# Kernel tuning notes

Measured on AMD Instinct MI355X. Metric: run time of the kernel, lower is better.

Reference implementation:

```python
import jax, jax.numpy as jnp
import numpy as np

NUM_SEGMENTS = 24  # static max number of sentence segments (matches segment_ids fill_max)


def setup_inputs() -> dict:
    key = jax.random.key(0)
    k1, k2, k3 = jax.random.split(key, 3)
    B, L, S, D = 32, 4, 512, 768
    embeddings = jax.random.normal(k1, (B, L, S, D), dtype=jnp.float32)
    # word index of each subword token (sorted, as produced by left-to-right '##' merging)
    token_group_ids = jnp.sort(jax.random.randint(k2, (B, S), 0, 300), axis=1).astype(jnp.int32)
    # sentence-segment id of each (aggregated) word position (sorted, from '.'-cumsum)
    segment_ids = jnp.sort(jax.random.randint(k3, (B, S), 0, NUM_SEGMENTS), axis=1).astype(jnp.int32)
    return {"embeddings": embeddings, "token_group_ids": token_group_ids, "segment_ids": segment_ids}


def _segsum(data, seg_ids, num_segments):
    # data: [S, D], seg_ids: [S] -> [num_segments, D]
    return jax.ops.segment_sum(data, seg_ids, num_segments=num_segments)


def reference(embeddings, token_group_ids, segment_ids):
    B, L, S, D = embeddings.shape
    # --- aggregate_tokens: scatter-sum subword embeddings into word slots, padded to S ---
    # vmap over batch and layer; word capacity = S (original pads agg_embs back to num_words)
    per_layer = jax.vmap(_segsum, in_axes=(0, None, None))          # over L
    per_batch = jax.vmap(per_layer, in_axes=(0, 0, None))           # over B
    word_layer = per_batch(embeddings, token_group_ids, S)          # [B, L, S, D]
    # --- sentence embedding: mean over (padded) word axis, then sum over layers ---
    sent_embeddings = word_layer.mean(axis=2).sum(axis=1)           # [B, D]
    # --- word embedding: sum over layers (aggregate_method='sum') ---
    word_embeddings = word_layer.sum(axis=1)                        # [B, S, D]
    # --- aggregate_segments: scatter-sum word embeddings into sentence segments ---
    seg_embeddings = jax.vmap(_segsum, in_axes=(0, 0, None))(
        word_embeddings, segment_ids, NUM_SEGMENTS)                 # [B, G, D]
    seg_num = segment_ids.max(axis=1) + 1                           # [B]
    seg_mask = jnp.arange(NUM_SEGMENTS)[None, :] >= seg_num[:, None]  # True = padded segment
    return word_embeddings, sent_embeddings, seg_embeddings, seg_mask
```

## Files before the change

kernel.cpp:

```cpp
#include <hip/hip_runtime.h>

#define BB 32
#define LL 4
#define SS 512
#define DD 768
#define D4 (DD / 4)
#define GG 24

typedef float floatx4 __attribute__((ext_vector_type(4)));

#define WB_STRIDE (SS + 1)
#define SB_STRIDE (GG + 1)

__global__ __launch_bounds__(SS) void bounds_kernel(
    const int* __restrict__ tg, const int* __restrict__ sg,
    int* __restrict__ wb, int* __restrict__ sb)
{
    __shared__ int ltg[SS];
    __shared__ int lsg[SS];
    const int b = blockIdx.x;
    const int t = threadIdx.x;
    ltg[t] = tg[b * SS + t];
    lsg[t] = sg[b * SS + t];
    __syncthreads();

    {
        int v = t, lo = 0, hi = SS;
        while (lo < hi) { int m = (lo + hi) >> 1; if (ltg[m] < v) lo = m + 1; else hi = m; }
        wb[b * WB_STRIDE + t] = lo;
        if (t == 0) wb[b * WB_STRIDE + SS] = SS;
    }
    if (t <= GG) {
        int v = t, lo = 0, hi = SS;
        while (lo < hi) { int m = (lo + hi) >> 1; if (lsg[m] < v) lo = m + 1; else hi = m; }
        sb[b * SB_STRIDE + t] = lo;
    }
}

__global__ __launch_bounds__(D4) void word_agg_kernel(
    const floatx4* __restrict__ emb, const int* __restrict__ wb, floatx4* __restrict__ word)
{
    const int g = blockIdx.x;
    const int b = blockIdx.y;
    const int lo = wb[b * WB_STRIDE + g];
    const int hi = wb[b * WB_STRIDE + g + 1];
    const int d = threadIdx.x;

    floatx4 acc = (floatx4)(0.f);
    for (int s = lo; s < hi; ++s) {
#pragma unroll
        for (int l = 0; l < LL; ++l) {
            floatx4 v = __builtin_nontemporal_load(
                &emb[((size_t)((b * LL + l) * SS + s)) * D4 + d]);
            acc += v;
        }
    }
    word[((size_t)(b * SS + g)) * D4 + d] = acc;
}

__global__ __launch_bounds__(D4) void seg_agg_kernel(
    const floatx4* __restrict__ word, const int* __restrict__ sb, floatx4* __restrict__ seg)
{
    const int t = blockIdx.x;
    const int b = blockIdx.y;
    const int lo = sb[b * SB_STRIDE + t];
    const int hi = sb[b * SB_STRIDE + t + 1];
    const int d = threadIdx.x;

    floatx4 acc = (floatx4)(0.f);
    for (int g = lo; g < hi; ++g) {
        acc += word[((size_t)(b * SS + g)) * D4 + d];
    }
    seg[((size_t)(b * GG + t)) * D4 + d] = acc;
}

__global__ __launch_bounds__(D4) void sent_mask_kernel(
    const floatx4* __restrict__ seg, const int* __restrict__ sg,
    floatx4* __restrict__ sent, float* __restrict__ mask)
{
    const int b = blockIdx.x;
    const int d = threadIdx.x;

    floatx4 acc = (floatx4)(0.f);
#pragma unroll
    for (int t = 0; t < GG; ++t) {
        acc += seg[((size_t)(b * GG + t)) * D4 + d];
    }
    acc *= (1.0f / (float)SS);
    sent[(size_t)b * D4 + d] = acc;

    if (d < GG) {
        const int seg_num = sg[b * SS + (SS - 1)] + 1;
        mask[b * GG + d] = (d >= seg_num) ? 1.0f : 0.0f;
    }
}

extern "C" void kernel_launch(void* const* d_in, const int* in_sizes, int n_in,
                              void* d_out, int out_size, void* d_ws, size_t ws_size,
                              hipStream_t stream) {
    const float* emb = (const float*)d_in[0];
    const int*   tg  = (const int*)d_in[1];
    const int*   sg  = (const int*)d_in[2];

    float* out  = (float*)d_out;
    float* word = out;
    float* sent = word + (size_t)BB * SS * DD;
    float* seg  = sent + (size_t)BB * DD;
    float* mask = seg  + (size_t)BB * GG * DD;

    int* wb = (int*)d_ws;
    int* sb = wb + BB * WB_STRIDE;

    bounds_kernel<<<BB, SS, 0, stream>>>(tg, sg, wb, sb);
    word_agg_kernel<<<dim3(SS, BB), D4, 0, stream>>>((const floatx4*)emb, wb, (floatx4*)word);
    seg_agg_kernel<<<dim3(GG, BB), D4, 0, stream>>>((const floatx4*)word, sb, (floatx4*)seg);
    sent_mask_kernel<<<BB, D4, 0, stream>>>((const floatx4*)seg, sg, (floatx4*)sent, mask);
}
```

Measured before the change: 299.5 us.

## Fuse word and segment aggregation into one kernel, move mask to bounds kernel

Combines the word-level and segment-level scatter-sum kernels into one. Each block handles one sentence segment, loops over its words, writes each word row and keeps a running segment sum in registers. This removes re-reading the word output from memory and saves a kernel launch. The padding-mask write moves into the bounds kernel. The cost is far fewer blocks (768 instead of 16384) with a long serial loop each, which can lower memory-level parallelism and cause load imbalance across segments.

```diff
diff --git a/kernel.cpp b/kernel.cpp
--- a/kernel.cpp
+++ b/kernel.cpp
@@ -14,7 +14,7 @@
 
 __global__ __launch_bounds__(SS) void bounds_kernel(
     const int* __restrict__ tg, const int* __restrict__ sg,
-    int* __restrict__ wb, int* __restrict__ sb)
+    int* __restrict__ wb, int* __restrict__ sb, float* __restrict__ mask)
 {
     __shared__ int ltg[SS];
     __shared__ int lsg[SS];
@@ -35,64 +35,53 @@
         while (lo < hi) { int m = (lo + hi) >> 1; if (lsg[m] < v) lo = m + 1; else hi = m; }
         sb[b * SB_STRIDE + t] = lo;
     }
+    if (t < GG) {
+        const int seg_num = lsg[SS - 1] + 1;
+        mask[b * GG + t] = (t >= seg_num) ? 1.0f : 0.0f;
+    }
 }
 
-__global__ __launch_bounds__(D4) void word_agg_kernel(
-    const floatx4* __restrict__ emb, const int* __restrict__ wb, floatx4* __restrict__ word)
-{
-    const int g = blockIdx.x;
-    const int b = blockIdx.y;
-    const int lo = wb[b * WB_STRIDE + g];
-    const int hi = wb[b * WB_STRIDE + g + 1];
-    const int d = threadIdx.x;
-
-    floatx4 acc = (floatx4)(0.f);
-    for (int s = lo; s < hi; ++s) {
-#pragma unroll
-        for (int l = 0; l < LL; ++l) {
-            floatx4 v = __builtin_nontemporal_load(
-                &emb[((size_t)((b * LL + l) * SS + s)) * D4 + d]);
-            acc += v;
-        }
-    }
-    word[((size_t)(b * SS + g)) * D4 + d] = acc;
-}
-
-__global__ __launch_bounds__(D4) void seg_agg_kernel(
-    const floatx4* __restrict__ word, const int* __restrict__ sb, floatx4* __restrict__ seg)
+__global__ __launch_bounds__(D4) void fused_agg_kernel(
+    const floatx4* __restrict__ emb, const int* __restrict__ wb,
+    const int* __restrict__ sb,
+    floatx4* __restrict__ word, floatx4* __restrict__ seg)
 {
     const int t = blockIdx.x;
     const int b = blockIdx.y;
-    const int lo = sb[b * SB_STRIDE + t];
-    const int hi = sb[b * SB_STRIDE + t + 1];
     const int d = threadIdx.x;
+    const int glo = sb[b * SB_STRIDE + t];
+    const int ghi = sb[b * SB_STRIDE + t + 1];
 
-    floatx4 acc = (floatx4)(0.f);
-    for (int g = lo; g < hi; ++g) {
-        acc += word[((size_t)(b * SS + g)) * D4 + d];
+    floatx4 seg_acc = (floatx4)(0.0f);
+    for (int g = glo; g < ghi; ++g) {
+        const int lo = wb[b * WB_STRIDE + g];
+        const int hi = wb[b * WB_STRIDE + g + 1];
+        floatx4 wacc = (floatx4)(0.0f);
+        for (int s = lo; s < hi; ++s) {
+#pragma unroll
+            for (int l = 0; l < LL; ++l) {
+                wacc += __builtin_nontemporal_load(
+                    &emb[((size_t)((b * LL + l) * SS + s)) * D4 + d]);
+            }
+        }
+        word[((size_t)(b * SS + g)) * D4 + d] = wacc;
+        seg_acc += wacc;
     }
-    seg[((size_t)(b * GG + t)) * D4 + d] = acc;
+    seg[((size_t)(b * GG + t)) * D4 + d] = seg_acc;
 }
 
-__global__ __launch_bounds__(D4) void sent_mask_kernel(
-    const floatx4* __restrict__ seg, const int* __restrict__ sg,
-    floatx4* __restrict__ sent, float* __restrict__ mask)
+__global__ __launch_bounds__(D4) void sent_kernel(
+    const floatx4* __restrict__ seg, floatx4* __restrict__ sent)
 {
     const int b = blockIdx.x;
     const int d = threadIdx.x;
-
-    floatx4 acc = (floatx4)(0.f);
+    floatx4 acc = (floatx4)(0.0f);
 #pragma unroll
     for (int t = 0; t < GG; ++t) {
         acc += seg[((size_t)(b * GG + t)) * D4 + d];
     }
     acc *= (1.0f / (float)SS);
     sent[(size_t)b * D4 + d] = acc;
-
-    if (d < GG) {
-        const int seg_num = sg[b * SS + (SS - 1)] + 1;
-        mask[b * GG + d] = (d >= seg_num) ? 1.0f : 0.0f;
-    }
 }
 
 extern "C" void kernel_launch(void* const* d_in, const int* in_sizes, int n_in,
@@ -111,8 +100,8 @@
     int* wb = (int*)d_ws;
     int* sb = wb + BB * WB_STRIDE;
 
-    bounds_kernel<<<BB, SS, 0, stream>>>(tg, sg, wb, sb);
-    word_agg_kernel<<<dim3(SS, BB), D4, 0, stream>>>((const floatx4*)emb, wb, (floatx4*)word);
-    seg_agg_kernel<<<dim3(GG, BB), D4, 0, stream>>>((const floatx4*)word, sb, (floatx4*)seg);
-    sent_mask_kernel<<<BB, D4, 0, stream>>>((const floatx4*)seg, sg, (floatx4*)sent, mask);
+    bounds_kernel<<<BB, SS, 0, stream>>>(tg, sg, wb, sb, mask);
+    fused_agg_kernel<<<dim3(GG, BB), D4, 0, stream>>>(
+        (const floatx4*)emb, wb, sb, (floatx4*)word, (floatx4*)seg);
+    sent_kernel<<<BB, D4, 0, stream>>>((const floatx4*)seg, (floatx4*)sent);
 }
```

Result: no change. 302.7 us (+1.1%).
